# Performance work log

Hardware: AMD Instinct MI355X
Metric: run time of the kernel (lower is better)

The kernel has to match this reference:

```python
import jax, jax.numpy as jnp
import numpy as np

B, S, D, BS = 256, 256, 448, 32
NB = D // BS  # 14 diagonal blocks


def setup_inputs() -> dict:
    key = jax.random.key(0)
    ks = jax.random.split(key, 9)
    xavier = float(np.sqrt(6.0 / (D + D)))
    inp = {
        "x": jax.random.normal(ks[0], (B, S, D), jnp.float32),
        "W_q": jax.random.uniform(ks[1], (D, D), jnp.float32, -xavier, xavier),
        "W_k": jax.random.uniform(ks[2], (D, D), jnp.float32, -xavier, xavier),
        "W_v": jax.random.uniform(ks[3], (D, D), jnp.float32, -xavier, xavier),
        "W_o": jax.random.uniform(ks[4], (D, D), jnp.float32, -xavier, xavier),
        "SSM_A": jnp.tril(jax.random.normal(ks[5], (D, D), jnp.float32) * 0.001),
        "SSM_B": jnp.tril(jax.random.normal(ks[6], (D, D), jnp.float32) * 0.001),
        "SSM_C": jnp.tril(jax.random.normal(ks[7], (D, D), jnp.float32) * 0.001),
        "dynamic_weight": jnp.full((1,), 0.5, jnp.float32),  # torch init value
        "ln_gamma": jnp.ones((D,), jnp.float32),
        "ln_beta": jnp.zeros((D,), jnp.float32),
    }
    return inp


def _diag_blocks(M):
    # extract the NB diagonal 32x32 blocks: [NB, BS, BS]
    idx = jnp.arange(NB)
    return M.reshape(NB, BS, NB, BS)[idx, :, idx, :]


def _block_linear(x, M):
    # block-diagonal matmul, vectorized over all 14 blocks at once
    xr = x.reshape(B, S, NB, BS)
    return jnp.einsum('bsni,nij->bsnj', xr, _diag_blocks(M)).reshape(B, S, D)


def _block_quadratic(x, M):
    # einsum('bsi,ij,bsk->bsj') per block == (x_blk @ M_blk) * sum_k(x_blk) * 0.1
    xr = x.reshape(B, S, NB, BS)
    y = jnp.einsum('bsni,nij->bsnj', xr, _diag_blocks(M))
    y = y * (jnp.sum(xr, axis=-1, keepdims=True) * 0.1)
    return y.reshape(B, S, D)


def _layer_norm(x, gamma, beta):
    mu = jnp.mean(x, axis=-1, keepdims=True)
    var = jnp.mean(jnp.square(x - mu), axis=-1, keepdims=True)
    return (x - mu) * jax.lax.rsqrt(var + 1e-5) * gamma + beta


def reference(x, W_q, W_k, W_v, W_o, SSM_A, SSM_B, SSM_C, dynamic_weight, ln_gamma, ln_beta):
    q = jnp.einsum('bsi,id->bsd', x, W_q)
    k = jnp.einsum('bsi,id->bsd', x, W_k)
    v = jnp.einsum('bsi,id->bsd', x, W_v)
    dw = jax.nn.sigmoid(dynamic_weight)  # sigmoid(0.5)=0.622 -> blended branch (seq_len == threshold)
    ssm_lin = _layer_norm(
        _block_linear(q, SSM_A) + _block_linear(k, SSM_B) + _block_linear(v, SSM_C),
        ln_gamma, ln_beta)
    ssm_quad = _layer_norm(
        _block_quadratic(q, SSM_A) + _block_quadratic(k, SSM_B) + _block_quadratic(v, SSM_C),
        ln_gamma, ln_beta)
    ssm = dw * ssm_quad + (1.0 - dw) * ssm_lin
    ssm = ssm + x  # residual; dropout is identity in eval mode
    return jnp.einsum('bsd,do->bso', ssm, W_o)
```

## Files before the change

kernel.cpp:

```cpp
#include <hip/hip_runtime.h>
#include <hip/hip_bf16.h>


typedef unsigned short u16;
typedef unsigned int u32;
typedef __bf16 bf16x8 __attribute__((ext_vector_type(8)));
typedef float f32x4 __attribute__((ext_vector_type(4)));

#define D_DIM 448
#define M_DIM 65536
#define NCAT 1386
#define NCAT_PAD 1408
#define N2_PAD 512

__device__ __forceinline__ u16 f2bf(float f) {
    union { float f; u32 u; } v; v.f = f;
    u32 u = v.u;
    u32 r = (u + 0x7fffu + ((u >> 16) & 1u)) >> 16;
    return (u16)r;
}
__device__ __forceinline__ float bf2f(u16 h) {
    union { u32 u; float f; } v; v.u = ((u32)h) << 16;
    return v.f;
}

__device__ __forceinline__ void load_lds16(const void* g, void* l) {
    __builtin_amdgcn_global_load_lds(
        (const __attribute__((address_space(1))) void*)g,
        (__attribute__((address_space(3))) void*)l, 16, 0, 0);
}

__global__ __launch_bounds__(64) void prep_wcat(
    const float* __restrict__ Wq, const float* __restrict__ Wk, const float* __restrict__ Wv,
    const float* __restrict__ SA, const float* __restrict__ SB, const float* __restrict__ SC,
    u16* __restrict__ WcatT)
{
    const int j = blockIdx.x;
    const int lane = threadIdx.x;
    u16* dst = WcatT + (size_t)j * D_DIM;

    if (j >= NCAT) {
        for (int t = lane; t < D_DIM; t += 64) dst[t] = 0;
        return;
    }
    if (j < 3 * D_DIM) {
        const int g = j / D_DIM, jj = j % D_DIM, n = jj >> 5;
        const float* W = (g == 0) ? Wq : (g == 1) ? Wk : Wv;
        const float* Mm = (g == 0) ? SA : (g == 1) ? SB : SC;
        __shared__ float av[32];
        if (lane < 32) av[lane] = Mm[(size_t)(n * 32 + lane) * D_DIM + jj];
        __syncthreads();
        for (int t = lane; t < D_DIM; t += 64) {
            const float* wrow = W + (size_t)t * D_DIM + n * 32;
            float s = 0.f;
            #pragma unroll
            for (int l = 0; l < 32; ++l) s += wrow[l] * av[l];
            dst[t] = f2bf(s);
        }
    } else {
        const int js = j - 3 * D_DIM;
        const int g = js / 14, n = js % 14;
        const float* W = (g == 0) ? Wq : (g == 1) ? Wk : Wv;
        for (int t = lane; t < D_DIM; t += 64) {
            const float* wrow = W + (size_t)t * D_DIM + n * 32;
            float s = 0.f;
            #pragma unroll
            for (int l = 0; l < 32; ++l) s += wrow[l];
            dst[t] = f2bf(0.1f * s);
        }
    }
}

__global__ __launch_bounds__(256) void prep_wo(const float* __restrict__ Wo, u16* __restrict__ WoT) {
    const int idx = blockIdx.x * 256 + threadIdx.x;
    const int o = idx / D_DIM, d = idx % D_DIM;
    WoT[idx] = (o < D_DIM) ? f2bf(Wo[(size_t)d * D_DIM + o]) : (u16)0;
}

__global__ __launch_bounds__(256) void cvt_x_kernel(const float* __restrict__ x, u16* __restrict__ xb) {
    const size_t i = ((size_t)blockIdx.x * 256 + threadIdx.x) * 4;
    float4 v = *reinterpret_cast<const float4*>(x + i);
    u16 o0 = f2bf(v.x), o1 = f2bf(v.y), o2 = f2bf(v.z), o3 = f2bf(v.w);
    u32 lo = (u32)o0 | ((u32)o1 << 16);
    u32 hi = (u32)o2 | ((u32)o3 << 16);
    u32* p = reinterpret_cast<u32*>(xb + i);
    p[0] = lo; p[1] = hi;
}

template<bool BF16OUT>
__global__ __launch_bounds__(256) void gemm_bt(
    const u16* __restrict__ A,
    const u16* __restrict__ Bt,
    void* __restrict__ Cout,
    int ldc, int nreal)
{
    __shared__ u16 lA[128 * 32];
    __shared__ u16 lB[128 * 32];
    const int tid = threadIdx.x;
    const int wave = tid >> 6, lane = tid & 63;
    const int brow = blockIdx.y * 128;
    const int bcol = blockIdx.x * 128;
    const int wr = wave >> 1, wc = wave & 1;

    f32x4 acc[4][4];
    #pragma unroll
    for (int i = 0; i < 4; ++i)
        #pragma unroll
        for (int j = 0; j < 4; ++j) {
            f32x4 z = {0.f, 0.f, 0.f, 0.f};
            acc[i][j] = z;
        }

    const int lrow = lane & 15;
    const int kgrp = (lane >> 4) << 3;

    for (int kt = 0; kt < 14; ++kt) {
        const int k0 = kt * 32;
        #pragma unroll
        for (int i = 0; i < 2; ++i) {
            const int chunk = (wave * 2 + i) * 64 + lane;
            const int row = chunk >> 2, kk = (chunk & 3) << 3;
            load_lds16(A + (size_t)(brow + row) * D_DIM + k0 + kk,
                       lA + (size_t)(wave * 2 + i) * 64 * 8);
            load_lds16(Bt + (size_t)(bcol + row) * D_DIM + k0 + kk,
                       lB + (size_t)(wave * 2 + i) * 64 * 8);
        }
        __syncthreads();

        bf16x8 af[4];
        #pragma unroll
        for (int mi = 0; mi < 4; ++mi) {
            const int r = wr * 64 + mi * 16 + lrow;
            af[mi] = *reinterpret_cast<const bf16x8*>(&lA[r * 32 + kgrp]);
        }
        #pragma unroll
        for (int ni = 0; ni < 4; ++ni) {
            const int n = wc * 64 + ni * 16 + lrow;
            bf16x8 bfr = *reinterpret_cast<const bf16x8*>(&lB[n * 32 + kgrp]);
            #pragma unroll
            for (int mi = 0; mi < 4; ++mi)
                acc[mi][ni] = __builtin_amdgcn_mfma_f32_16x16x32_bf16(af[mi], bfr, acc[mi][ni], 0, 0, 0);
        }
        __syncthreads();
    }

    const int rbase = brow + wr * 64 + ((lane >> 4) << 2);
    const int cbase = bcol + wc * 64 + (lane & 15);
    #pragma unroll
    for (int mi = 0; mi < 4; ++mi) {
        #pragma unroll
        for (int ni = 0; ni < 4; ++ni) {
            const int col = cbase + ni * 16;
            #pragma unroll
            for (int r = 0; r < 4; ++r) {
                const int row = rbase + mi * 16 + r;
                const float v = acc[mi][ni][r];
                if (BF16OUT) {
                    ((u16*)Cout)[(size_t)row * ldc + col] = f2bf(v);
                } else {
                    if (col < nreal)
                        ((float*)Cout)[(size_t)row * nreal + col] = v;
                }
            }
        }
    }
}

__global__ __launch_bounds__(256) void ssm_epilogue(
    const u16* __restrict__ Z, const float* __restrict__ x,
    const float* __restrict__ gamma, const float* __restrict__ beta,
    const float* __restrict__ dynw, u16* __restrict__ ssm)
{
    const int row = blockIdx.x * 4 + (threadIdx.x >> 6);
    const int lane = threadIdx.x & 63;
    const u16* zr = Z + (size_t)row * NCAT_PAD;
    const float dwv = 1.0f / (1.0f + __expf(-dynw[0]));

    float lin[7], quad[7];
    float s0 = 0.f, s1 = 0.f, s2 = 0.f, s3 = 0.f;
    #pragma unroll
    for (int i = 0; i < 7; ++i) {
        const int j = lane + (i << 6);
        const int n = j >> 5;
        const float a = bf2f(zr[j]);
        const float b = bf2f(zr[448 + j]);
        const float c = bf2f(zr[896 + j]);
        const float sA = bf2f(zr[1344 + n]);
        const float sB = bf2f(zr[1358 + n]);
        const float sC = bf2f(zr[1372 + n]);
        const float L = a + b + c;
        const float Q = a * sA + b * sB + c * sC;
        lin[i] = L; quad[i] = Q;
        s0 += L; s1 += L * L; s2 += Q; s3 += Q * Q;
    }
    #pragma unroll
    for (int off = 32; off > 0; off >>= 1) {
        s0 += __shfl_xor(s0, off);
        s1 += __shfl_xor(s1, off);
        s2 += __shfl_xor(s2, off);
        s3 += __shfl_xor(s3, off);
    }
    const float inv = 1.0f / 448.0f;
    const float mu0 = s0 * inv, mu1 = s2 * inv;
    const float rs0 = rsqrtf(fmaxf(s1 * inv - mu0 * mu0, 0.f) + 1e-5f);
    const float rs1 = rsqrtf(fmaxf(s3 * inv - mu1 * mu1, 0.f) + 1e-5f);

    #pragma unroll
    for (int i = 0; i < 7; ++i) {
        const int j = lane + (i << 6);
        const float g = gamma[j], bt = beta[j];
        const float ln = (lin[i] - mu0) * rs0 * g + bt;
        const float qn = (quad[i] - mu1) * rs1 * g + bt;
        const float v = dwv * qn + (1.0f - dwv) * ln + x[(size_t)row * D_DIM + j];
        ssm[(size_t)row * D_DIM + j] = f2bf(v);
    }
}

extern "C" void kernel_launch(void* const* d_in, const int* in_sizes, int n_in,
                              void* d_out, int out_size, void* d_ws, size_t ws_size,
                              hipStream_t stream) {
    const float* x    = (const float*)d_in[0];
    const float* Wq   = (const float*)d_in[1];
    const float* Wk   = (const float*)d_in[2];
    const float* Wv   = (const float*)d_in[3];
    const float* Wo   = (const float*)d_in[4];
    const float* SA   = (const float*)d_in[5];
    const float* SB   = (const float*)d_in[6];
    const float* SC   = (const float*)d_in[7];
    const float* dynw = (const float*)d_in[8];
    const float* gma  = (const float*)d_in[9];
    const float* bta  = (const float*)d_in[10];
    float* out = (float*)d_out;

    char* ws = (char*)d_ws;
    u16* Xbf   = (u16*)(ws);
    u16* WcatT = (u16*)(ws + 58720256);
    u16* WoT   = (u16*)(ws + 59981824);
    u16* Z     = (u16*)(ws + 60440576);

    prep_wcat<<<dim3(NCAT_PAD), dim3(64), 0, stream>>>(Wq, Wk, Wv, SA, SB, SC, WcatT);
    prep_wo<<<dim3(896), dim3(256), 0, stream>>>(Wo, WoT);
    cvt_x_kernel<<<dim3(28672), dim3(256), 0, stream>>>(x, Xbf);

    gemm_bt<true><<<dim3(NCAT_PAD / 128, M_DIM / 128), dim3(256), 0, stream>>>(
        Xbf, WcatT, (void*)Z, NCAT_PAD, NCAT_PAD);

    ssm_epilogue<<<dim3(M_DIM / 4), dim3(256), 0, stream>>>(Z, x, gma, bta, dynw, Xbf);

    gemm_bt<false><<<dim3(N2_PAD / 128, M_DIM / 128), dim3(256), 0, stream>>>(
        Xbf, WoT, (void*)out, 448, 448);
}
```

Baseline: 483.7 us.

## Use 64-wide K steps, XCD-aware block remap, and vectorized SSM epilogue

The GEMM now loads two 32-wide K slices per barrier pair, halving the number of synchronizations per tile. It also uses a 1D grid whose block indices are remapped so consecutive tiles land on the same XCD (bid&7 striping) for better L2 reuse. The epilogue is vectorized to 8 contiguous elements per lane with 16-byte loads and stores, and the block scale sums are fetched once and broadcast with shuffles. The residual now reads the bf16 copy of x instead of fp32 x, which adds a little rounding error in exchange for less memory traffic.

```diff
diff --git a/kernel.cpp b/kernel.cpp
--- a/kernel.cpp
+++ b/kernel.cpp
@@ -92,14 +92,18 @@
     const u16* __restrict__ A,
     const u16* __restrict__ Bt,
     void* __restrict__ Cout,
-    int ldc, int nreal)
+    int ldc, int nreal, int ncolblk)
 {
-    __shared__ u16 lA[128 * 32];
-    __shared__ u16 lB[128 * 32];
+    __shared__ u16 lA[2][128 * 32];
+    __shared__ u16 lB[2][128 * 32];
     const int tid = threadIdx.x;
     const int wave = tid >> 6, lane = tid & 63;
-    const int brow = blockIdx.y * 128;
-    const int bcol = blockIdx.x * 128;
+
+    const int cpx = gridDim.x >> 3;
+    const int bid = blockIdx.x;
+    const int t = (bid & 7) * cpx + (bid >> 3);
+    const int bx = t % ncolblk, by = t / ncolblk;
+    const int brow = by * 128, bcol = bx * 128;
     const int wr = wave >> 1, wc = wave & 1;
 
     f32x4 acc[4][4];
@@ -114,32 +118,39 @@
     const int lrow = lane & 15;
     const int kgrp = (lane >> 4) << 3;
 
-    for (int kt = 0; kt < 14; ++kt) {
-        const int k0 = kt * 32;
-        #pragma unroll
-        for (int i = 0; i < 2; ++i) {
-            const int chunk = (wave * 2 + i) * 64 + lane;
-            const int row = chunk >> 2, kk = (chunk & 3) << 3;
-            load_lds16(A + (size_t)(brow + row) * D_DIM + k0 + kk,
-                       lA + (size_t)(wave * 2 + i) * 64 * 8);
-            load_lds16(Bt + (size_t)(bcol + row) * D_DIM + k0 + kk,
-                       lB + (size_t)(wave * 2 + i) * 64 * 8);
+    for (int kt = 0; kt < 7; ++kt) {
+        const int k0 = kt * 64;
+        #pragma unroll
+        for (int ks = 0; ks < 2; ++ks) {
+            const int kb = k0 + ks * 32;
+            #pragma unroll
+            for (int i = 0; i < 2; ++i) {
+                const int chunk = (wave * 2 + i) * 64 + lane;
+                const int row = chunk >> 2, kk = (chunk & 3) << 3;
+                load_lds16(A + (size_t)(brow + row) * D_DIM + kb + kk,
+                           &lA[ks][(wave * 2 + i) * 512]);
+                load_lds16(Bt + (size_t)(bcol + row) * D_DIM + kb + kk,
+                           &lB[ks][(wave * 2 + i) * 512]);
+            }
         }
         __syncthreads();
 
-        bf16x8 af[4];
-        #pragma unroll
-        for (int mi = 0; mi < 4; ++mi) {
-            const int r = wr * 64 + mi * 16 + lrow;
-            af[mi] = *reinterpret_cast<const bf16x8*>(&lA[r * 32 + kgrp]);
-        }
-        #pragma unroll
-        for (int ni = 0; ni < 4; ++ni) {
-            const int n = wc * 64 + ni * 16 + lrow;
-            bf16x8 bfr = *reinterpret_cast<const bf16x8*>(&lB[n * 32 + kgrp]);
-            #pragma unroll
-            for (int mi = 0; mi < 4; ++mi)
-                acc[mi][ni] = __builtin_amdgcn_mfma_f32_16x16x32_bf16(af[mi], bfr, acc[mi][ni], 0, 0, 0);
+        #pragma unroll
+        for (int ks = 0; ks < 2; ++ks) {
+            bf16x8 af[4];
+            #pragma unroll
+            for (int mi = 0; mi < 4; ++mi) {
+                const int r = wr * 64 + mi * 16 + lrow;
+                af[mi] = *reinterpret_cast<const bf16x8*>(&lA[ks][r * 32 + kgrp]);
+            }
+            #pragma unroll
+            for (int ni = 0; ni < 4; ++ni) {
+                const int n = wc * 64 + ni * 16 + lrow;
+                bf16x8 bfr = *reinterpret_cast<const bf16x8*>(&lB[ks][n * 32 + kgrp]);
+                #pragma unroll
+                for (int mi = 0; mi < 4; ++mi)
+                    acc[mi][ni] = __builtin_amdgcn_mfma_f32_16x16x32_bf16(af[mi], bfr, acc[mi][ni], 0, 0, 0);
+            }
         }
         __syncthreads();
     }
@@ -167,7 +178,7 @@
 }
 
 __global__ __launch_bounds__(256) void ssm_epilogue(
-    const u16* __restrict__ Z, const float* __restrict__ x,
+    const u16* __restrict__ Z, const u16* __restrict__ xb,
     const float* __restrict__ gamma, const float* __restrict__ beta,
     const float* __restrict__ dynw, u16* __restrict__ ssm)
 {
@@ -175,23 +186,41 @@
     const int lane = threadIdx.x & 63;
     const u16* zr = Z + (size_t)row * NCAT_PAD;
     const float dwv = 1.0f / (1.0f + __expf(-dynw[0]));
-
-    float lin[7], quad[7];
+    const bool act = lane < 56;
+    const int j0 = lane * 8;
+    const int n = lane >> 2;
+
+    float sv = (lane < 42) ? bf2f(zr[1344 + lane]) : 0.f;
+    const float sA = __shfl(sv, n);
+    const float sB = __shfl(sv, 14 + n);
+    const float sC = __shfl(sv, 28 + n);
+
+    float L[8], Q[8];
     float s0 = 0.f, s1 = 0.f, s2 = 0.f, s3 = 0.f;
-    #pragma unroll
-    for (int i = 0; i < 7; ++i) {
-        const int j = lane + (i << 6);
-        const int n = j >> 5;
-        const float a = bf2f(zr[j]);
-        const float b = bf2f(zr[448 + j]);
-        const float c = bf2f(zr[896 + j]);
-        const float sA = bf2f(zr[1344 + n]);
-        const float sB = bf2f(zr[1358 + n]);
-        const float sC = bf2f(zr[1372 + n]);
-        const float L = a + b + c;
-        const float Q = a * sA + b * sB + c * sC;
-        lin[i] = L; quad[i] = Q;
-        s0 += L; s1 += L * L; s2 += Q; s3 += Q * Q;
+    if (act) {
+        uint4 va = *reinterpret_cast<const uint4*>(zr + j0);
+        uint4 vb = *reinterpret_cast<const uint4*>(zr + 448 + j0);
+        uint4 vc = *reinterpret_cast<const uint4*>(zr + 896 + j0);
+        const u32* pa = reinterpret_cast<const u32*>(&va);
+        const u32* pb = reinterpret_cast<const u32*>(&vb);
+        const u32* pc = reinterpret_cast<const u32*>(&vc);
+        #pragma unroll
+        for (int w = 0; w < 4; ++w) {
+            #pragma unroll
+            for (int h = 0; h < 2; ++h) {
+                const int i = w * 2 + h;
+                const float a = bf2f((u16)((pa[w] >> (16 * h)) & 0xffffu));
+                const float b = bf2f((u16)((pb[w] >> (16 * h)) & 0xffffu));
+                const float c = bf2f((u16)((pc[w] >> (16 * h)) & 0xffffu));
+                const float Lv = a + b + c;
+                const float Qv = a * sA + b * sB + c * sC;
+                L[i] = Lv; Q[i] = Qv;
+                s0 += Lv; s1 += Lv * Lv; s2 += Qv; s3 += Qv * Qv;
+            }
+        }
+    } else {
+        #pragma unroll
+        for (int i = 0; i < 8; ++i) { L[i] = 0.f; Q[i] = 0.f; }
     }
     #pragma unroll
     for (int off = 32; off > 0; off >>= 1) {
@@ -205,14 +234,39 @@
     const float rs0 = rsqrtf(fmaxf(s1 * inv - mu0 * mu0, 0.f) + 1e-5f);
     const float rs1 = rsqrtf(fmaxf(s3 * inv - mu1 * mu1, 0.f) + 1e-5f);
 
-    #pragma unroll
-    for (int i = 0; i < 7; ++i) {
-        const int j = lane + (i << 6);
-        const float g = gamma[j], bt = beta[j];
-        const float ln = (lin[i] - mu0) * rs0 * g + bt;
-        const float qn = (quad[i] - mu1) * rs1 * g + bt;
-        const float v = dwv * qn + (1.0f - dwv) * ln + x[(size_t)row * D_DIM + j];
-        ssm[(size_t)row * D_DIM + j] = f2bf(v);
+    if (act) {
+        float4 g0 = *reinterpret_cast<const float4*>(gamma + j0);
+        float4 g1 = *reinterpret_cast<const float4*>(gamma + j0 + 4);
+        float4 b0 = *reinterpret_cast<const float4*>(beta + j0);
+        float4 b1 = *reinterpret_cast<const float4*>(beta + j0 + 4);
+        const float* gp = &g0.x;
+        float gv[8] = {g0.x, g0.y, g0.z, g0.w, g1.x, g1.y, g1.z, g1.w};
+        float bv[8] = {b0.x, b0.y, b0.z, b0.w, b1.x, b1.y, b1.z, b1.w};
+        (void)gp;
+        uint4 vx = *reinterpret_cast<const uint4*>(xb + (size_t)row * D_DIM + j0);
+        const u32* px = reinterpret_cast<const u32*>(&vx);
+        u32 outw[4];
+        #pragma unroll
+        for (int w = 0; w < 4; ++w) {
+            u16 h0, h1;
+            {
+                const int i = w * 2;
+                const float xr = bf2f((u16)(px[w] & 0xffffu));
+                const float ln = (L[i] - mu0) * rs0 * gv[i] + bv[i];
+                const float qn = (Q[i] - mu1) * rs1 * gv[i] + bv[i];
+                h0 = f2bf(dwv * qn + (1.0f - dwv) * ln + xr);
+            }
+            {
+                const int i = w * 2 + 1;
+                const float xr = bf2f((u16)(px[w] >> 16));
+                const float ln = (L[i] - mu0) * rs0 * gv[i] + bv[i];
+                const float qn = (Q[i] - mu1) * rs1 * gv[i] + bv[i];
+                h1 = f2bf(dwv * qn + (1.0f - dwv) * ln + xr);
+            }
+            outw[w] = (u32)h0 | ((u32)h1 << 16);
+        }
+        uint4 ov = {outw[0], outw[1], outw[2], outw[3]};
+        *reinterpret_cast<uint4*>(ssm + (size_t)row * D_DIM + j0) = ov;
     }
 }
 
@@ -242,11 +296,11 @@
     prep_wo<<<dim3(896), dim3(256), 0, stream>>>(Wo, WoT);
     cvt_x_kernel<<<dim3(28672), dim3(256), 0, stream>>>(x, Xbf);
 
-    gemm_bt<true><<<dim3(NCAT_PAD / 128, M_DIM / 128), dim3(256), 0, stream>>>(
-        Xbf, WcatT, (void*)Z, NCAT_PAD, NCAT_PAD);
-
-    ssm_epilogue<<<dim3(M_DIM / 4), dim3(256), 0, stream>>>(Z, x, gma, bta, dynw, Xbf);
-
-    gemm_bt<false><<<dim3(N2_PAD / 128, M_DIM / 128), dim3(256), 0, stream>>>(
-        Xbf, WoT, (void*)out, 448, 448);
-}
+    gemm_bt<true><<<dim3(5632), dim3(256), 0, stream>>>(
+        Xbf, WcatT, (void*)Z, NCAT_PAD, NCAT_PAD, 11);
+
+    ssm_epilogue<<<dim3(M_DIM / 4), dim3(256), 0, stream>>>(Z, Xbf, gma, bta, dynw, Xbf);
+
+    gemm_bt<false><<<dim3(2048), dim3(256), 0, stream>>>(
+        Xbf, WoT, (void*)out, 448, 448, 4);
+}
```

New measurement: 449.0 us. 1.08x faster.
